# Kernel tuning notes

Measured on AMD Instinct MI355X. Metric: run time of the kernel, lower is better.

## Reference

```python
import jax, jax.numpy as jnp
import numpy as np

N, F_DIM, H_DIM = 8192, 128, 128

def setup_inputs() -> dict:
    key = jax.random.key(0)
    ks = jax.random.split(key, 7)
    inp = {
        "input": jax.random.normal(ks[0], (N, F_DIM), dtype=jnp.float32),
        "wavelets": jax.random.normal(ks[1], (N, N), dtype=jnp.float32) / np.sqrt(N),
        "wavelets_inv": jax.random.normal(ks[2], (N, N), dtype=jnp.float32) / np.sqrt(N),
        # layer 1 params
        "W1": jax.random.uniform(ks[3], (F_DIM, H_DIM), dtype=jnp.float32,
                                 minval=-np.sqrt(6.0/(F_DIM+H_DIM)), maxval=np.sqrt(6.0/(F_DIM+H_DIM))),
        "f1": jax.random.uniform(ks[4], (N,), dtype=jnp.float32, minval=0.9, maxval=1.1),
        # layer 2 params
        "W2": jax.random.uniform(ks[5], (H_DIM, H_DIM), dtype=jnp.float32,
                                 minval=-np.sqrt(6.0/(H_DIM+H_DIM)), maxval=np.sqrt(6.0/(H_DIM+H_DIM))),
        "f2": jax.random.uniform(ks[6], (N,), dtype=jnp.float32, minval=0.9, maxval=1.1),
    }
    return inp

def _gwnn_layer(features, wavelets, wavelets_inv, W, filt):
    # torch: wavelets @ diag(filt) @ (wavelets_inv @ (features @ W))
    # diag(filt) matmul == column-wise scale of wavelets (broadcast elementwise)
    xw = features @ W                      # [N, out]
    spec = wavelets_inv @ xw               # [N, out] spectral-domain features
    spec = filt[:, None] * spec            # apply learnable diagonal filter
    return wavelets @ spec                 # [N, out]

def reference(input, wavelets, wavelets_inv, W1, f1, W2, f2):
    # eval mode: dropout is identity
    h1 = jax.nn.relu(_gwnn_layer(input, wavelets, wavelets_inv, W1, f1))
    out = _gwnn_layer(h1, wavelets, wavelets_inv, W2, f2)
    return out
```

## Files before the change

### kernel.cpp

```cpp
#include <hip/hip_runtime.h>
#include <hip/hip_bf16.h>
#include <stdint.h>


typedef __attribute__((ext_vector_type(4))) float f32x4;
typedef __attribute__((ext_vector_type(8))) short s16x8;
typedef __attribute__((ext_vector_type(4))) short s16x4;

#define DEVI static __device__ __forceinline__

DEVI short bf1(float x){ __bf16 h = (__bf16)x; return __builtin_bit_cast(short, h); }

DEVI s16x8 cvt8(f32x4 lo, f32x4 hi){
  s16x8 r;
#pragma unroll
  for (int i = 0; i < 4; ++i){ r[i] = bf1(lo[i]); r[4+i] = bf1(hi[i]); }
  return r;
}

DEVI void glds16(const void* g, void* l){
  __builtin_amdgcn_global_load_lds((const __attribute__((address_space(1))) void*)g,
                                   (__attribute__((address_space(3))) void*)l, 16, 0, 0);
}

template<int N> DEVI void waitvm(){
  if constexpr (N == 0)       asm volatile("s_waitcnt vmcnt(0)"  ::: "memory");
  else if constexpr (N == 5)  asm volatile("s_waitcnt vmcnt(5)"  ::: "memory");
  else if constexpr (N == 6)  asm volatile("s_waitcnt vmcnt(6)"  ::: "memory");
  else if constexpr (N == 12) asm volatile("s_waitcnt vmcnt(12)" ::: "memory");
}

__global__ __launch_bounds__(256, 1) void gemm_big(
    const float* __restrict__ Ap, const short* __restrict__ Btp,
    float* __restrict__ Pp, int K, int M)
{
  constexpr int BM = 128, BK = 64;
  constexpr int ASZ = BM*BK*4;
  constexpr int BSZ = 128*BK*2;
  constexpr int TSZ = ASZ + BSZ;
  constexpr int NBUF = 3, PRE = 2;
  __shared__ uint8_t lds[NBUF*TSZ];

  const int tid  = threadIdx.x;
  const int lane = tid & 63;
  const int wv   = tid >> 6;
  const int la   = lane & 15;
  const int g4   = lane >> 4;
  const int m0   = blockIdx.x * BM;
  const int kq   = blockIdx.y;
  const int K4   = K >> 2;
  const int kb   = kq * K4;

  const float* gAbase = Ap + (size_t)m0*K + kb;
  int aoffg[8];
#pragma unroll
  for (int j = 0; j < 8; ++j){
    const int rl = (wv<<5) + (j<<2) + (lane>>4);
    aoffg[j] = rl*K + (((lane&15) ^ (rl&15))<<2);
  }

  const int nb0 = (wv<<5) + (lane>>3);
  const short* gB0 = Btp + (size_t)(nb0    )*K + kb + (((lane&7)^(nb0&7))<<3);
  const short* gB1 = Btp + (size_t)(nb0+ 8 )*K + kb + (((lane&7)^(nb0&7))<<3);
  const short* gB2 = Btp + (size_t)(nb0+16 )*K + kb + (((lane&7)^(nb0&7))<<3);
  const short* gB3 = Btp + (size_t)(nb0+24 )*K + kb + (((lane&7)^(nb0&7))<<3);

  int aoff[2][2][2];
#pragma unroll
  for (int mi = 0; mi < 2; ++mi){
    const int r = (wv<<5) + mi*16 + la;
#pragma unroll
    for (int kf = 0; kf < 2; ++kf){
      const int v0 = kf*8 + (g4<<1);
      aoff[mi][kf][0] = r*256 + (((v0  )^(r&15))<<4);
      aoff[mi][kf][1] = r*256 + (((v0+1)^(r&15))<<4);
    }
  }
  int boff[8][2];
#pragma unroll
  for (int ni = 0; ni < 8; ++ni){
    const int n = ni*16 + la;
#pragma unroll
    for (int kf = 0; kf < 2; ++kf){
      const int u = kf*4 + g4;
      boff[ni][kf] = n*128 + ((u^(n&7))<<4);
    }
  }

  f32x4 acc[2][8] = {};

  int kk = 0;
  uint8_t* const lend = lds + NBUF*TSZ;
  uint8_t* bs = lds;
  uint8_t* bc = lds;

  auto STAGE = [&](){
    uint8_t* Ab = bs;
    uint8_t* Bb = bs + ASZ;
#pragma unroll
    for (int j = 0; j < 8; ++j)
      glds16(gAbase + aoffg[j] + kk, Ab + (wv<<13) + (j<<10));
    kk += BK;
    glds16(gB0, Bb + (wv<<12));
    glds16(gB1, Bb + (wv<<12) + 1024);
    glds16(gB2, Bb + (wv<<12) + 2048);
    glds16(gB3, Bb + (wv<<12) + 3072);
    gB0 += BK; gB1 += BK; gB2 += BK; gB3 += BK;
    bs += TSZ; if (bs == lend) bs = lds;
  };

  auto COMPUTE = [&](){
    const uint8_t* Ab = bc;
    const uint8_t* Bb = bc + ASZ;
#pragma unroll
    for (int kf = 0; kf < 2; ++kf){
      s16x8 a0 = cvt8(*(const f32x4*)(Ab + aoff[0][kf][0]),
                      *(const f32x4*)(Ab + aoff[0][kf][1]));
      s16x8 a1 = cvt8(*(const f32x4*)(Ab + aoff[1][kf][0]),
                      *(const f32x4*)(Ab + aoff[1][kf][1]));
#pragma unroll
      for (int ni = 0; ni < 8; ++ni){
        s16x8 b = *(const s16x8*)(Bb + boff[ni][kf]);
        acc[0][ni] = __builtin_amdgcn_mfma_f32_16x16x32_bf16(a0, b, acc[0][ni], 0, 0, 0);
        acc[1][ni] = __builtin_amdgcn_mfma_f32_16x16x32_bf16(a1, b, acc[1][ni], 0, 0, 0);
      }
    }
    bc += TSZ; if (bc == lend) bc = lds;
  };

  const int ns = K4 >> 6;
  for (int s = 0; s < PRE && s < ns; ++s) STAGE();

  for (int t = 0; t < ns; ++t){
    if (t < ns - 1) waitvm<12>();
    else            waitvm<0>();
    __builtin_amdgcn_s_barrier();
    asm volatile("" ::: "memory");
    if (t + PRE < ns) STAGE();
    COMPUTE();
    asm volatile("" ::: "memory");
  }

  float* P = Pp + (size_t)kq * M * 128;
  const int rbase = m0 + (wv<<5) + (g4<<2);
#pragma unroll
  for (int mi = 0; mi < 2; ++mi)
#pragma unroll
    for (int ni = 0; ni < 8; ++ni)
#pragma unroll
      for (int r = 0; r < 4; ++r)
        P[(size_t)(rbase + mi*16 + r)*128 + ni*16 + la] = acc[mi][ni][r];
}

template<bool ABF>
__global__ __launch_bounds__(256, 1) void sgemm(
    const void* __restrict__ Ap, const short* __restrict__ Btp,
    void* __restrict__ Outp, int K, int M)
{
  constexpr int BM = 32, BN = 128, BK = 64;
  constexpr int ASZ = ABF ? BM*BK*2 : BM*BK*4;
  constexpr int BSZ = BN*BK*2;
  constexpr int TSZ = ASZ + BSZ;
  constexpr int NL  = ABF ? 5 : 6;
  constexpr int NBUF = 3, PRE = 2;
  __shared__ uint8_t lds[NBUF*TSZ];

  const int tid  = threadIdx.x;
  const int lane = tid & 63;
  const int wv   = tid >> 6;
  const int la   = lane & 15;
  const int g4   = lane >> 4;
  const int m0   = blockIdx.x * BM;

  const float* gA0 = nullptr; const float* gA1 = nullptr; const short* gAh = nullptr;
  if constexpr (!ABF){
    const float* Af = (const float*)Ap;
    int r0 = (wv<<3) + (lane>>4);
    int r1 = r0 + 4;
    gA0 = Af + (size_t)(m0+r0)*K + (((lane&15)^(r0&15))<<2);
    gA1 = Af + (size_t)(m0+r1)*K + (((lane&15)^(r1&15))<<2);
  } else {
    const short* Ah = (const short*)Ap;
    int r = (wv<<3) + (lane>>3);
    gAh = Ah + (size_t)(m0+r)*K + (((lane&7)^(r&7))<<3);
  }
  const int nb0 = (wv<<5) + (lane>>3);
  const short* gB0 = Btp + (size_t)(nb0    )*K + (((lane&7)^(nb0&7))<<3);
  const short* gB1 = Btp + (size_t)(nb0+ 8 )*K + (((lane&7)^(nb0&7))<<3);
  const short* gB2 = Btp + (size_t)(nb0+16 )*K + (((lane&7)^(nb0&7))<<3);
  const short* gB3 = Btp + (size_t)(nb0+24 )*K + (((lane&7)^(nb0&7))<<3);

  int aoff[2][2][2];
  int boff[2][2];
#pragma unroll
  for (int mi = 0; mi < 2; ++mi){
    const int r = mi*16 + la;
#pragma unroll
    for (int kf = 0; kf < 2; ++kf){
      if constexpr (!ABF){
        const int v0 = kf*8 + (g4<<1);
        aoff[mi][kf][0] = r*256 + (((v0  )^(r&15))<<4);
        aoff[mi][kf][1] = r*256 + (((v0+1)^(r&15))<<4);
      } else {
        const int u = kf*4 + g4;
        aoff[mi][kf][0] = r*128 + ((u^(r&7))<<4);
        aoff[mi][kf][1] = 0;
      }
    }
  }
#pragma unroll
  for (int ni = 0; ni < 2; ++ni){
    const int n = (wv<<5) + ni*16 + la;
#pragma unroll
    for (int kf = 0; kf < 2; ++kf){
      const int u = kf*4 + g4;
      boff[ni][kf] = n*128 + ((u^(n&7))<<4);
    }
  }

  f32x4 acc[2][2] = {};

  auto STAGE = [&](uint8_t* buf){
    uint8_t* Ab = buf;
    uint8_t* Bb = buf + ASZ;
    if constexpr (!ABF){
      glds16(gA0, Ab + (wv<<11));
      glds16(gA1, Ab + (wv<<11) + 1024);
      gA0 += BK; gA1 += BK;
    } else {
      glds16(gAh, Ab + (wv<<10));
      gAh += BK;
    }
    glds16(gB0, Bb + (wv<<12));
    glds16(gB1, Bb + (wv<<12) + 1024);
    glds16(gB2, Bb + (wv<<12) + 2048);
    glds16(gB3, Bb + (wv<<12) + 3072);
    gB0 += BK; gB1 += BK; gB2 += BK; gB3 += BK;
  };

  auto COMPUTE = [&](const uint8_t* buf){
    const uint8_t* Ab = buf;
    const uint8_t* Bb = buf + ASZ;
#pragma unroll
    for (int kf = 0; kf < 2; ++kf){
      s16x8 a0, a1, b0, b1;
      if constexpr (!ABF){
        a0 = cvt8(*(const f32x4*)(Ab + aoff[0][kf][0]), *(const f32x4*)(Ab + aoff[0][kf][1]));
        a1 = cvt8(*(const f32x4*)(Ab + aoff[1][kf][0]), *(const f32x4*)(Ab + aoff[1][kf][1]));
      } else {
        a0 = *(const s16x8*)(Ab + aoff[0][kf][0]);
        a1 = *(const s16x8*)(Ab + aoff[1][kf][0]);
      }
      b0 = *(const s16x8*)(Bb + boff[0][kf]);
      b1 = *(const s16x8*)(Bb + boff[1][kf]);
      acc[0][0] = __builtin_amdgcn_mfma_f32_16x16x32_bf16(a0, b0, acc[0][0], 0, 0, 0);
      acc[0][1] = __builtin_amdgcn_mfma_f32_16x16x32_bf16(a0, b1, acc[0][1], 0, 0, 0);
      acc[1][0] = __builtin_amdgcn_mfma_f32_16x16x32_bf16(a1, b0, acc[1][0], 0, 0, 0);
      acc[1][1] = __builtin_amdgcn_mfma_f32_16x16x32_bf16(a1, b1, acc[1][1], 0, 0, 0);
    }
  };

  const int ns = K >> 6;
  uint8_t* const lend = lds + NBUF*TSZ;
  uint8_t* bs = lds;
  uint8_t* bc = lds;
  for (int s = 0; s < PRE && s < ns; ++s){
    STAGE(bs);
    bs += TSZ; if (bs == lend) bs = lds;
  }
  for (int t = 0; t < ns; ++t){
    if (t < ns - 1) waitvm<NL>(); else waitvm<0>();
    __builtin_amdgcn_s_barrier();
    asm volatile("" ::: "memory");
    if (t + PRE < ns){
      STAGE(bs);
      bs += TSZ; if (bs == lend) bs = lds;
    }
    COMPUTE(bc);
    bc += TSZ; if (bc == lend) bc = lds;
    asm volatile("" ::: "memory");
  }

  const int mbase = m0 + (g4<<2);
  const int nc0   = (wv<<5) + la;
#pragma unroll
  for (int mi = 0; mi < 2; ++mi){
#pragma unroll
    for (int ni = 0; ni < 2; ++ni){
      s16x4 pk;
#pragma unroll
      for (int r = 0; r < 4; ++r) pk[r] = bf1(acc[mi][ni][r]);
      *(s16x4*)((short*)Outp + (size_t)(nc0 + (ni<<4))*M + (mbase + (mi<<4))) = pk;
    }
  }
}


__global__ __launch_bounds__(256) void red_t(
    const float* __restrict__ Pp, const float* __restrict__ fp,
    short* __restrict__ out, int M)
{
  __shared__ short t[128*65];
  const size_t S = (size_t)M*128;
  const int m0 = blockIdx.x * 64;
  const int tid = threadIdx.x;
#pragma unroll
  for (int it = 0; it < 8; ++it){
    const int idx = it*256 + tid;
    const int m = idx >> 5, nq = idx & 31;
    const float* base = Pp + (size_t)(m0+m)*128;
    f32x4 a = ((const f32x4*)(base      ))[nq];
    f32x4 b = ((const f32x4*)(base +   S))[nq];
    f32x4 c = ((const f32x4*)(base + 2*S))[nq];
    f32x4 d = ((const f32x4*)(base + 3*S))[nq];
    const float fv = fp[m0+m];
#pragma unroll
    for (int j = 0; j < 4; ++j)
      t[(nq*4+j)*65 + m] = bf1(fv * ((a[j] + b[j]) + (c[j] + d[j])));
  }
  __syncthreads();
#pragma unroll
  for (int it = 0; it < 8; ++it){
    const int idx = it*256 + tid;
    const int n = idx >> 4, mc = idx & 15;
    s16x4 v;
#pragma unroll
    for (int j = 0; j < 4; ++j) v[j] = t[n*65 + mc*4 + j];
    *(s16x4*)(out + (size_t)n*M + m0 + mc*4) = v;
  }
}

__global__ __launch_bounds__(256) void red_r(
    const float* __restrict__ Pp, short* __restrict__ out, int M)
{
  const size_t S = (size_t)M*128;
  const size_t i0 = (size_t)(blockIdx.x*256 + threadIdx.x) * 8;
  s16x8 v;
#pragma unroll
  for (int h = 0; h < 2; ++h){
    f32x4 a = *(const f32x4*)(Pp + i0 + 4*h);
    f32x4 b = *(const f32x4*)(Pp + i0 + 4*h + S);
    f32x4 c = *(const f32x4*)(Pp + i0 + 4*h + 2*S);
    f32x4 d = *(const f32x4*)(Pp + i0 + 4*h + 3*S);
#pragma unroll
    for (int j = 0; j < 4; ++j)
      v[4*h+j] = bf1(fmaxf((a[j] + b[j]) + (c[j] + d[j]), 0.0f));
  }
  *(s16x8*)(out + i0) = v;
}

__global__ __launch_bounds__(256) void red_f(
    const float* __restrict__ Pp, float* __restrict__ out, int M)
{
  const size_t S = (size_t)M*128;
  const size_t i0 = (size_t)(blockIdx.x*256 + threadIdx.x) * 4;
  f32x4 a = *(const f32x4*)(Pp + i0);
  f32x4 b = *(const f32x4*)(Pp + i0 + S);
  f32x4 c = *(const f32x4*)(Pp + i0 + 2*S);
  f32x4 d = *(const f32x4*)(Pp + i0 + 3*S);
  *(f32x4*)(out + i0) = (a + b) + (c + d);
}

__global__ void wtrans_k(const float* __restrict__ W1, const float* __restrict__ W2,
                         short* __restrict__ T1, short* __restrict__ T2){
  const int idx = blockIdx.x*256 + threadIdx.x;
  const int m = idx >> 14, rem = idx & 16383;
  const int n = rem >> 7, k = rem & 127;
  const float* W = m ? W2 : W1;
  short* T = m ? T2 : T1;
  T[n*128 + k] = bf1(W[k*128 + n]);
}

extern "C" void kernel_launch(void* const* d_in, const int* in_sizes, int n_in,
                              void* d_out, int out_size, void* d_ws, size_t ws_size,
                              hipStream_t stream){
  const float* input = (const float*)d_in[0];
  const float* wav   = (const float*)d_in[1];
  const float* winv  = (const float*)d_in[2];
  const float* W1    = (const float*)d_in[3];
  const float* f1    = (const float*)d_in[4];
  const float* W2    = (const float*)d_in[5];
  const float* f2    = (const float*)d_in[6];

  constexpr int M = 8192;
  uint8_t* ws = (uint8_t*)d_ws;
  short* W1T = (short*)(ws);
  short* W2T = (short*)(ws + (32<<10));
  short* XWT = (short*)(ws + (64<<10));
  short* SPT = (short*)(ws + (64<<10) + (2<<20));
  short* H1  = (short*)(ws + (64<<10) + (4<<20));
  float* P   = (float*)(ws + (64<<10) + (6<<20));

  dim3 b(256);
  dim3 gbig(M/128, 4);
  dim3 gns(M/32);
  dim3 grt(M/64);
  dim3 grr(M*128/(256*8));
  dim3 grf(M*128/(256*4));
  dim3 gt(128);

  wtrans_k<<<gt, b, 0, stream>>>(W1, W2, W1T, W2T);
  sgemm<false><<<gns, b, 0, stream>>>(input, W1T, XWT, 128, M);
  gemm_big<<<gbig, b, 0, stream>>>(winv, XWT, P, M, M);
  red_t  <<<grt, b, 0, stream>>>(P, f1, SPT, M);
  gemm_big<<<gbig, b, 0, stream>>>(wav, SPT, P, M, M);
  red_r  <<<grr, b, 0, stream>>>(P, H1, M);
  sgemm<true ><<<gns, b, 0, stream>>>(H1, W2T, XWT, 128, M);
  gemm_big<<<gbig, b, 0, stream>>>(winv, XWT, P, M, M);
  red_t  <<<grt, b, 0, stream>>>(P, f2, SPT, M);
  gemm_big<<<gbig, b, 0, stream>>>(wav, SPT, P, M, M);
  red_f  <<<grf, b, 0, stream>>>(P, (float*)d_out, M);
}
```

Baseline: 306.9 us.

## Cache bf16 copies of wavelet matrices during layer-1 GEMMs for reuse in layer 2

The first-layer big GEMMs now write a bf16 copy of the fp32 wavelet matrix A as they convert it for MFMA. The second-layer GEMMs read these half-size copies, using a deeper LDS pipeline and adjusted vmcnt waits. This halves A read traffic in layer 2 but adds a full bf16 write of each 8192x8192 matrix in layer 1. The path only runs if the workspace is large enough.

```diff
diff --git a/kernel.cpp b/kernel.cpp
--- a/kernel.cpp
+++ b/kernel.cpp
@@ -27,18 +27,23 @@
   if constexpr (N == 0)       asm volatile("s_waitcnt vmcnt(0)"  ::: "memory");
   else if constexpr (N == 5)  asm volatile("s_waitcnt vmcnt(5)"  ::: "memory");
   else if constexpr (N == 6)  asm volatile("s_waitcnt vmcnt(6)"  ::: "memory");
+  else if constexpr (N == 8)  asm volatile("s_waitcnt vmcnt(8)"  ::: "memory");
   else if constexpr (N == 12) asm volatile("s_waitcnt vmcnt(12)" ::: "memory");
-}
-
+  else if constexpr (N == 16) asm volatile("s_waitcnt vmcnt(16)" ::: "memory");
+  else if constexpr (N == 20) asm volatile("s_waitcnt vmcnt(20)" ::: "memory");
+}
+
+template<bool ABF, bool WCOPY>
 __global__ __launch_bounds__(256, 1) void gemm_big(
-    const float* __restrict__ Ap, const short* __restrict__ Btp,
-    float* __restrict__ Pp, int K, int M)
+    const void* __restrict__ Ap, const short* __restrict__ Btp,
+    float* __restrict__ Pp, short* __restrict__ Acp, int K, int M)
 {
   constexpr int BM = 128, BK = 64;
-  constexpr int ASZ = BM*BK*4;
+  constexpr int ASZ = ABF ? BM*BK*2 : BM*BK*4;
   constexpr int BSZ = 128*BK*2;
   constexpr int TSZ = ASZ + BSZ;
-  constexpr int NBUF = 3, PRE = 2;
+  constexpr int NBUF = ABF ? 4 : 3;
+  constexpr int PRE  = ABF ? 3 : 2;
   __shared__ uint8_t lds[NBUF*TSZ];
 
   const int tid  = threadIdx.x;
@@ -51,12 +56,22 @@
   const int K4   = K >> 2;
   const int kb   = kq * K4;
 
-  const float* gAbase = Ap + (size_t)m0*K + kb;
+  const float* gAf = nullptr; const short* gAh = nullptr;
   int aoffg[8];
-#pragma unroll
-  for (int j = 0; j < 8; ++j){
-    const int rl = (wv<<5) + (j<<2) + (lane>>4);
-    aoffg[j] = rl*K + (((lane&15) ^ (rl&15))<<2);
+  if constexpr (!ABF){
+    gAf = (const float*)Ap + (size_t)m0*K + kb;
+#pragma unroll
+    for (int j = 0; j < 8; ++j){
+      const int rl = (wv<<5) + (j<<2) + (lane>>4);
+      aoffg[j] = rl*K + (((lane&15) ^ (rl&15))<<2);
+    }
+  } else {
+    gAh = (const short*)Ap + (size_t)m0*K + kb;
+#pragma unroll
+    for (int j = 0; j < 4; ++j){
+      const int rl = (wv<<5) + (j<<3) + (lane>>3);
+      aoffg[j] = rl*K + (((lane&7) ^ (rl&7))<<3);
+    }
   }
 
   const int nb0 = (wv<<5) + (lane>>3);
@@ -71,9 +86,15 @@
     const int r = (wv<<5) + mi*16 + la;
 #pragma unroll
     for (int kf = 0; kf < 2; ++kf){
-      const int v0 = kf*8 + (g4<<1);
-      aoff[mi][kf][0] = r*256 + (((v0  )^(r&15))<<4);
-      aoff[mi][kf][1] = r*256 + (((v0+1)^(r&15))<<4);
+      if constexpr (!ABF){
+        const int v0 = kf*8 + (g4<<1);
+        aoff[mi][kf][0] = r*256 + (((v0  )^(r&15))<<4);
+        aoff[mi][kf][1] = r*256 + (((v0+1)^(r&15))<<4);
+      } else {
+        const int u = kf*4 + g4;
+        aoff[mi][kf][0] = r*128 + ((u^(r&7))<<4);
+        aoff[mi][kf][1] = 0;
+      }
     }
   }
   int boff[8][2];
@@ -87,9 +108,14 @@
     }
   }
 
+  short* Acw = nullptr;
+  if constexpr (WCOPY)
+    Acw = Acp + (size_t)(m0 + (wv<<5) + la)*K + kb + (g4<<3);
+
   f32x4 acc[2][8] = {};
 
   int kk = 0;
+  int kc = 0;
   uint8_t* const lend = lds + NBUF*TSZ;
   uint8_t* bs = lds;
   uint8_t* bc = lds;
@@ -97,9 +123,15 @@
   auto STAGE = [&](){
     uint8_t* Ab = bs;
     uint8_t* Bb = bs + ASZ;
-#pragma unroll
-    for (int j = 0; j < 8; ++j)
-      glds16(gAbase + aoffg[j] + kk, Ab + (wv<<13) + (j<<10));
+    if constexpr (!ABF){
+#pragma unroll
+      for (int j = 0; j < 8; ++j)
+        glds16(gAf + aoffg[j] + kk, Ab + (wv<<13) + (j<<10));
+    } else {
+#pragma unroll
+      for (int j = 0; j < 4; ++j)
+        glds16(gAh + aoffg[j] + kk, Ab + (wv<<12) + (j<<10));
+    }
     kk += BK;
     glds16(gB0, Bb + (wv<<12));
     glds16(gB1, Bb + (wv<<12) + 1024);
@@ -114,10 +146,20 @@
     const uint8_t* Bb = bc + ASZ;
 #pragma unroll
     for (int kf = 0; kf < 2; ++kf){
-      s16x8 a0 = cvt8(*(const f32x4*)(Ab + aoff[0][kf][0]),
-                      *(const f32x4*)(Ab + aoff[0][kf][1]));
-      s16x8 a1 = cvt8(*(const f32x4*)(Ab + aoff[1][kf][0]),
-                      *(const f32x4*)(Ab + aoff[1][kf][1]));
+      s16x8 a0, a1;
+      if constexpr (!ABF){
+        a0 = cvt8(*(const f32x4*)(Ab + aoff[0][kf][0]),
+                  *(const f32x4*)(Ab + aoff[0][kf][1]));
+        a1 = cvt8(*(const f32x4*)(Ab + aoff[1][kf][0]),
+                  *(const f32x4*)(Ab + aoff[1][kf][1]));
+        if constexpr (WCOPY){
+          *(s16x8*)(Acw + kc + kf*32)            = a0;
+          *(s16x8*)(Acw + (size_t)16*K + kc + kf*32) = a1;
+        }
+      } else {
+        a0 = *(const s16x8*)(Ab + aoff[0][kf][0]);
+        a1 = *(const s16x8*)(Ab + aoff[1][kf][0]);
+      }
 #pragma unroll
       for (int ni = 0; ni < 8; ++ni){
         s16x8 b = *(const s16x8*)(Bb + boff[ni][kf]);
@@ -125,6 +167,7 @@
         acc[1][ni] = __builtin_amdgcn_mfma_f32_16x16x32_bf16(a1, b, acc[1][ni], 0, 0, 0);
       }
     }
+    kc += BK;
     bc += TSZ; if (bc == lend) bc = lds;
   };
 
@@ -132,8 +175,18 @@
   for (int s = 0; s < PRE && s < ns; ++s) STAGE();
 
   for (int t = 0; t < ns; ++t){
-    if (t < ns - 1) waitvm<12>();
-    else            waitvm<0>();
+    if constexpr (ABF){
+      if (t <= ns - 3)      waitvm<16>();
+      else if (t == ns - 2) waitvm<8>();
+      else                  waitvm<0>();
+    } else if constexpr (WCOPY){
+      if (t == 0)           waitvm<12>();
+      else if (t == 1)      waitvm<16>();
+      else if (t <= ns - 2) waitvm<20>();
+      else                  waitvm<8>();
+    } else {
+      if (t < ns - 1) waitvm<12>(); else waitvm<0>();
+    }
     __builtin_amdgcn_s_barrier();
     asm volatile("" ::: "memory");
     if (t + PRE < ns) STAGE();
@@ -390,6 +443,10 @@
   short* SPT = (short*)(ws + (64<<10) + (2<<20));
   short* H1  = (short*)(ws + (64<<10) + (4<<20));
   float* P   = (float*)(ws + (64<<10) + (6<<20));
+  short* WI16 = (short*)(ws + (64<<10) + (22<<20));
+  short* WA16 = WI16 + (size_t)M*M;
+  const size_t needed = (64<<10) + (size_t)(22<<20) + 2*(size_t)M*M*2;
+  const bool big = (ws_size >= needed);
 
   dim3 b(256);
   dim3 gbig(M/128, 4);
@@ -401,13 +458,25 @@
 
   wtrans_k<<<gt, b, 0, stream>>>(W1, W2, W1T, W2T);
   sgemm<false><<<gns, b, 0, stream>>>(input, W1T, XWT, 128, M);
-  gemm_big<<<gbig, b, 0, stream>>>(winv, XWT, P, M, M);
-  red_t  <<<grt, b, 0, stream>>>(P, f1, SPT, M);
-  gemm_big<<<gbig, b, 0, stream>>>(wav, SPT, P, M, M);
-  red_r  <<<grr, b, 0, stream>>>(P, H1, M);
-  sgemm<true ><<<gns, b, 0, stream>>>(H1, W2T, XWT, 128, M);
-  gemm_big<<<gbig, b, 0, stream>>>(winv, XWT, P, M, M);
-  red_t  <<<grt, b, 0, stream>>>(P, f2, SPT, M);
-  gemm_big<<<gbig, b, 0, stream>>>(wav, SPT, P, M, M);
-  red_f  <<<grf, b, 0, stream>>>(P, (float*)d_out, M);
-}
+  if (big){
+    gemm_big<false,true ><<<gbig, b, 0, stream>>>(winv, XWT, P, WI16, M, M);
+    red_t<<<grt, b, 0, stream>>>(P, f1, SPT, M);
+    gemm_big<false,true ><<<gbig, b, 0, stream>>>(wav, SPT, P, WA16, M, M);
+    red_r<<<grr, b, 0, stream>>>(P, H1, M);
+    sgemm<true ><<<gns, b, 0, stream>>>(H1, W2T, XWT, 128, M);
+    gemm_big<true ,false><<<gbig, b, 0, stream>>>(WI16, XWT, P, nullptr, M, M);
+    red_t<<<grt, b, 0, stream>>>(P, f2, SPT, M);
+    gemm_big<true ,false><<<gbig, b, 0, stream>>>(WA16, SPT, P, nullptr, M, M);
+    red_f<<<grf, b, 0, stream>>>(P, (float*)d_out, M);
+  } else {
+    gemm_big<false,false><<<gbig, b, 0, stream>>>(winv, XWT, P, nullptr, M, M);
+    red_t<<<grt, b, 0, stream>>>(P, f1, SPT, M);
+    gemm_big<false,false><<<gbig, b, 0, stream>>>(wav, SPT, P, nullptr, M, M);
+    red_r<<<grr, b, 0, stream>>>(P, H1, M);
+    sgemm<true ><<<gns, b, 0, stream>>>(H1, W2T, XWT, 128, M);
+    gemm_big<false,false><<<gbig, b, 0, stream>>>(winv, XWT, P, nullptr, M, M);
+    red_t<<<grt, b, 0, stream>>>(P, f2, SPT, M);
+    gemm_big<false,false><<<gbig, b, 0, stream>>>(wav, SPT, P, nullptr, M, M);
+    red_f<<<grf, b, 0, stream>>>(P, (float*)d_out, M);
+  }
+}
```

Measured after the change: 354.8 us. +15.6%, slower.
